# Kernel tuning notes

Hardware: AMD Instinct MI355X
Metric: run time of the kernel (lower is better)

## Reference

```python
import jax, jax.numpy as jnp
import numpy as np

EPS = 1e-5  # torch LayerNorm default
NUM_HEADS = 16


def _ln(x, g, b):
    mu = x.mean(-1, keepdims=True)
    var = ((x - mu) ** 2).mean(-1, keepdims=True)
    return (x - mu) * jax.lax.rsqrt(var + EPS) * g + b


def _softmax1(logits):
    # softmax with an extra implicit zero logit appended on the last axis
    z = jnp.pad(logits, [(0, 0)] * (logits.ndim - 1) + [(0, 1)])
    return jax.nn.softmax(z, axis=-1)[..., :-1]


def setup_inputs() -> dict:
    key = jax.random.key(0)
    ks = jax.random.split(key, 8)
    B, N, C = 4, 1024, 1024
    Hd = 4 * C  # mlp hidden
    s = lambda k, shape, sc: (jax.random.normal(k, shape, jnp.float32) * sc)
    return {
        "x": s(ks[0], (B, N, C), 1.0),
        "mask": jax.random.bernoulli(ks[1], 0.1, (B, N, N)),  # True = masked
        "ln1_g": jnp.ones((C,), jnp.float32),
        "ln1_b": jnp.zeros((C,), jnp.float32),
        "qkv_w": s(ks[2], (3 * C, C), 0.02),
        "qkv_b": jnp.zeros((3 * C,), jnp.float32),
        "proj_w": s(ks[3], (C, C), 0.02),
        "proj_b": jnp.zeros((C,), jnp.float32),
        "ln2_g": jnp.ones((C,), jnp.float32),
        "ln2_b": jnp.zeros((C,), jnp.float32),
        "fc1_w": s(ks[4], (Hd, C), 0.02),
        "fc1_b": jnp.zeros((Hd,), jnp.float32),
        "fc2_w": s(ks[5], (C, Hd), 0.02),
        "fc2_b": jnp.zeros((C,), jnp.float32),
    }


def reference(x, mask, ln1_g, ln1_b, qkv_w, qkv_b, proj_w, proj_b,
              ln2_g, ln2_b, fc1_w, fc1_b, fc2_w, fc2_b):
    B, N, C = x.shape
    H = NUM_HEADS
    D = C // H
    scale = D ** (-0.5)
    # --- pre-norm attention ---
    h = _ln(x, ln1_g, ln1_b)
    qkv = (h @ qkv_w.T + qkv_b).reshape(B, N, 3, H, D).transpose(2, 0, 3, 1, 4)
    q, k, v = qkv[0], qkv[1], qkv[2]  # each [B,H,N,D]
    attn = jnp.einsum('bhqd,bhkd->bhqk', q, k) * scale
    attn = jnp.where(mask[:, None], -jnp.finfo(attn.dtype).max, attn)
    attn = _softmax1(attn)  # allow_zero_attn=True variant
    o = jnp.einsum('bhqk,bhkd->bqhd', attn, v).reshape(B, N, C)
    o = o @ proj_w.T + proj_b
    x = x + o
    # --- pre-norm MLP (exact GELU, matching torch nn.GELU default) ---
    h2 = _ln(x, ln2_g, ln2_b)
    m = jax.nn.gelu(h2 @ fc1_w.T + fc1_b, approximate=False)
    m = m @ fc2_w.T + fc2_b
    return x + m
```

## Files before the change

kernel.cpp:

```cpp
#include <hip/hip_runtime.h>
#include <hip/hip_bf16.h>
#include <cstdint>
#include <cstddef>

typedef __attribute__((ext_vector_type(4))) float f32x4;
typedef __attribute__((ext_vector_type(8))) short s16x8;
typedef __attribute__((ext_vector_type(4))) unsigned int u32x4;
typedef __attribute__((ext_vector_type(4))) unsigned short u16x4;

__device__ __forceinline__ unsigned short f2bf(float f) {
  union { float f; unsigned int u; } v; v.f = f;
  return (unsigned short)((v.u + 0x7fffu + ((v.u >> 16) & 1u)) >> 16);
}

__device__ __forceinline__ void gll16(const void* g, void* l) {
  __builtin_amdgcn_global_load_lds(
      (const __attribute__((address_space(1))) void*)g,
      (__attribute__((address_space(3))) void*)l, 16, 0, 0);
}

__global__ void mask_detect(const unsigned char* __restrict__ m, int* __restrict__ flag) {
  __shared__ int f;
  if (threadIdx.x == 0) f = 0;
  __syncthreads();
  unsigned int found = 0;
  for (int i = threadIdx.x * 16; i < 65536; i += 256 * 16) {
    u32x4 v = *(const u32x4*)(m + i);
    found |= (v.x & 0xFFFFFF00u) | (v.y & 0xFFFFFF00u) |
             (v.z & 0xFFFFFF00u) | (v.w & 0xFFFFFF00u);
  }
  if (found) atomicOr(&f, 1);
  __syncthreads();
  if (threadIdx.x == 0) *flag = f;
}

__global__ __launch_bounds__(256)
void ln_bf16(const float* __restrict__ x, const float* __restrict__ g,
             const float* __restrict__ bta, unsigned short* __restrict__ out) {
  const int row = blockIdx.x;
  const int t = threadIdx.x;
  const float* xr = x + (size_t)row * 1024;
  f32x4 v = *(const f32x4*)(xr + t * 4);
  float s  = v.x + v.y + v.z + v.w;
  float sq = v.x * v.x + v.y * v.y + v.z * v.z + v.w * v.w;
#pragma unroll
  for (int d = 1; d < 64; d <<= 1) { s += __shfl_xor(s, d, 64); sq += __shfl_xor(sq, d, 64); }
  __shared__ float ss[4], ssq[4];
  const int w = t >> 6;
  if ((t & 63) == 0) { ss[w] = s; ssq[w] = sq; }
  __syncthreads();
  s  = ss[0] + ss[1] + ss[2] + ss[3];
  sq = ssq[0] + ssq[1] + ssq[2] + ssq[3];
  const float mu  = s * (1.0f / 1024.0f);
  const float var = sq * (1.0f / 1024.0f) - mu * mu;
  const float rs  = rsqrtf(var + 1e-5f);
  f32x4 gv = *(const f32x4*)(g + t * 4);
  f32x4 bv = *(const f32x4*)(bta + t * 4);
  u16x4 o;
  o.x = f2bf((v.x - mu) * rs * gv.x + bv.x);
  o.y = f2bf((v.y - mu) * rs * gv.y + bv.y);
  o.z = f2bf((v.z - mu) * rs * gv.z + bv.z);
  o.w = f2bf((v.w - mu) * rs * gv.w + bv.w);
  *(u16x4*)(out + (size_t)row * 1024 + t * 4) = o;
}

__global__ __launch_bounds__(256)
void f32_to_bf16(const float* __restrict__ in, unsigned short* __restrict__ out, int n) {
  for (int i = (blockIdx.x * 256 + threadIdx.x) * 4; i < n; i += gridDim.x * 256 * 4) {
    f32x4 v = *(const f32x4*)(in + i);
    u16x4 o = { f2bf(v.x), f2bf(v.y), f2bf(v.z), f2bf(v.w) };
    *(u16x4*)(out + i) = o;
  }
}

template<int EPI>
__global__ __launch_bounds__(256)
void gemm_bt(const unsigned short* __restrict__ A, const unsigned short* __restrict__ Bw,
             const float* __restrict__ bias, const float* __restrict__ resid,
             void* __restrict__ Cout, int M, int N, int K) {
  __shared__ unsigned short As[128 * 64];
  __shared__ unsigned short Bs[128 * 64];
  const int tid = threadIdx.x;
  const int bx = blockIdx.x;
  const int by = blockIdx.y;
  const int w = tid >> 6, l = tid & 63;
  const int wr = w >> 1, wc = w & 1;
  const int lr = l & 15, lk = l >> 4;

  f32x4 acc[4][4] = {};
  const int row0A = by * 128, row0B = bx * 128;

  for (int kt = 0; kt < K; kt += 64) {
#pragma unroll
    for (int it = 0; it < 4; ++it) {
      const int c = it * 256 + tid;
      const int r = c >> 3, c8 = (c & 7) * 8;
      gll16(A  + (size_t)(row0A + r) * K + kt + c8, As + c * 8);
      gll16(Bw + (size_t)(row0B + r) * K + kt + c8, Bs + c * 8);
    }
    asm volatile("s_waitcnt vmcnt(0)" ::: "memory");
    __syncthreads();
#pragma unroll
    for (int ks = 0; ks < 2; ++ks) {
      s16x8 af[4], bfr[4];
#pragma unroll
      for (int m = 0; m < 4; ++m)
        af[m] = *(const s16x8*)&As[(wr * 64 + m * 16 + lr) * 64 + ks * 32 + lk * 8];
#pragma unroll
      for (int n = 0; n < 4; ++n)
        bfr[n] = *(const s16x8*)&Bs[(wc * 64 + n * 16 + lr) * 64 + ks * 32 + lk * 8];
#pragma unroll
      for (int m = 0; m < 4; ++m)
#pragma unroll
        for (int n = 0; n < 4; ++n)
          acc[m][n] = __builtin_amdgcn_mfma_f32_16x16x32_bf16(af[m], bfr[n], acc[m][n], 0, 0, 0);
    }
    __syncthreads();
  }
#pragma unroll
  for (int m = 0; m < 4; ++m) {
#pragma unroll
    for (int n = 0; n < 4; ++n) {
      const int col = bx * 128 + wc * 64 + n * 16 + lr;
      const float bval = bias[col];
#pragma unroll
      for (int r2 = 0; r2 < 4; ++r2) {
        const int row = by * 128 + wr * 64 + m * 16 + lk * 4 + r2;
        float vv = acc[m][n][r2] + bval;
        const size_t idx = (size_t)row * N + col;
        if (EPI == 0) {
          ((unsigned short*)Cout)[idx] = f2bf(vv);
        } else if (EPI == 1) {
          float ge = 0.5f * vv * (1.0f + erff(vv * 0.70710678118f));
          ((unsigned short*)Cout)[idx] = f2bf(ge);
        } else {
          ((float*)Cout)[idx] = vv + resid[idx];
        }
      }
    }
  }
}

__global__ __launch_bounds__(256)
void attn_kernel(const unsigned short* __restrict__ qkv, const void* __restrict__ maskp,
                 const int* __restrict__ flag, unsigned short* __restrict__ o_ws) {
  __shared__ unsigned short Qs[64 * 64];
  __shared__ unsigned short Ks[64 * 64];
  __shared__ unsigned short Vts[64 * 64];
  __shared__ unsigned short Ps[4][16 * 64];
  __shared__ __align__(16) unsigned char Ms[64 * 64];

  const int tid = threadIdx.x;
  const int bh = blockIdx.x, qt = blockIdx.y;
  const int b = bh >> 4, h = bh & 15;
  const int q0 = qt * 64;
  const int w = tid >> 6, l = tid & 63;
  const int lr = l & 15, lk = l >> 4;
  const size_t rowbase = (size_t)b * 1024;
  const int qoff = h * 64, koff = 1024 + h * 64, voff = 2048 + h * 64;

#pragma unroll
  for (int it = 0; it < 2; ++it) {
    const int c = it * 256 + tid;
    const int r = c >> 3, c8 = (c & 7) * 8;
    gll16(qkv + (rowbase + q0 + r) * 3072 + qoff + c8, Qs + c * 8);
  }
  const int mask_is_byte = *flag;

  float m_r[4] = {0.f, 0.f, 0.f, 0.f};
  float l_r[4] = {1.f, 1.f, 1.f, 1.f};
  f32x4 acc_o[4] = {};

  for (int nt = 0; nt < 16; ++nt) {
    const int n0 = nt * 64;
    __syncthreads();
#pragma unroll
    for (int it = 0; it < 2; ++it) {
      const int c = it * 256 + tid;
      const int r = c >> 3, c8 = (c & 7) * 8;
      gll16(qkv + (rowbase + n0 + r) * 3072 + koff + c8, Ks + c * 8);
    }
    {
      const int n = tid & 63, dg = tid >> 6;
      const u32x4* src = (const u32x4*)(qkv + (rowbase + n0 + n) * 3072 + voff + dg * 16);
      u32x4 v0 = src[0], v1 = src[1];
      const unsigned short* e0 = (const unsigned short*)&v0;
      const unsigned short* e1 = (const unsigned short*)&v1;
#pragma unroll
      for (int j = 0; j < 8; ++j) Vts[(dg * 16 + j) * 64 + n] = e0[j];
#pragma unroll
      for (int j = 0; j < 8; ++j) Vts[(dg * 16 + 8 + j) * 64 + n] = e1[j];
    }
    {
      const int r = tid >> 2, c16 = (tid & 3) * 16;
      const size_t moff = ((size_t)b * 1024 + q0 + r) * 1024 + n0 + c16;
      if (mask_is_byte) {
        *(u32x4*)&Ms[r * 64 + c16] = *(const u32x4*)((const unsigned char*)maskp + moff);
      } else {
        const int* mi = (const int*)maskp + moff;
#pragma unroll
        for (int j = 0; j < 16; ++j) Ms[r * 64 + c16 + j] = (mi[j] != 0) ? 1 : 0;
      }
    }
    asm volatile("s_waitcnt vmcnt(0)" ::: "memory");
    __syncthreads();

    f32x4 s_acc[4] = {};
#pragma unroll
    for (int ks = 0; ks < 2; ++ks) {
      s16x8 aq = *(const s16x8*)&Qs[(w * 16 + lr) * 64 + ks * 32 + lk * 8];
#pragma unroll
      for (int n = 0; n < 4; ++n) {
        s16x8 bk = *(const s16x8*)&Ks[(n * 16 + lr) * 64 + ks * 32 + lk * 8];
        s_acc[n] = __builtin_amdgcn_mfma_f32_16x16x32_bf16(aq, bk, s_acc[n], 0, 0, 0);
      }
    }
    float sv[4][4], pm[4];
#pragma unroll
    for (int r2 = 0; r2 < 4; ++r2) pm[r2] = -3.0e38f;
#pragma unroll
    for (int n = 0; n < 4; ++n)
#pragma unroll
      for (int r2 = 0; r2 < 4; ++r2) {
        float s = s_acc[n][r2] * 0.125f;
        const int qrow = w * 16 + lk * 4 + r2, kcol = n * 16 + lr;
        if (Ms[qrow * 64 + kcol]) s = -3.0e38f;
        sv[n][r2] = s;
        pm[r2] = fmaxf(pm[r2], s);
      }
#pragma unroll
    for (int d = 1; d < 16; d <<= 1)
#pragma unroll
      for (int r2 = 0; r2 < 4; ++r2) pm[r2] = fmaxf(pm[r2], __shfl_xor(pm[r2], d, 64));

    float resc[4], psum[4];
#pragma unroll
    for (int r2 = 0; r2 < 4; ++r2) {
      const float mnew = fmaxf(m_r[r2], pm[r2]);
      resc[r2] = __expf(m_r[r2] - mnew);
      m_r[r2] = mnew;
      psum[r2] = 0.f;
    }
#pragma unroll
    for (int n = 0; n < 4; ++n)
#pragma unroll
      for (int r2 = 0; r2 < 4; ++r2) {
        const float p = __expf(sv[n][r2] - m_r[r2]);
        psum[r2] += p;
        Ps[w][(lk * 4 + r2) * 64 + n * 16 + lr] = f2bf(p);
      }
#pragma unroll
    for (int d = 1; d < 16; d <<= 1)
#pragma unroll
      for (int r2 = 0; r2 < 4; ++r2) psum[r2] += __shfl_xor(psum[r2], d, 64);
#pragma unroll
    for (int r2 = 0; r2 < 4; ++r2) l_r[r2] = l_r[r2] * resc[r2] + psum[r2];
#pragma unroll
    for (int dn = 0; dn < 4; ++dn)
#pragma unroll
      for (int r2 = 0; r2 < 4; ++r2) acc_o[dn][r2] *= resc[r2];
#pragma unroll
    for (int ks = 0; ks < 2; ++ks) {
      s16x8 ap = *(const s16x8*)&Ps[w][lr * 64 + ks * 32 + lk * 8];
#pragma unroll
      for (int dn = 0; dn < 4; ++dn) {
        s16x8 bv = *(const s16x8*)&Vts[(dn * 16 + lr) * 64 + ks * 32 + lk * 8];
        acc_o[dn] = __builtin_amdgcn_mfma_f32_16x16x32_bf16(ap, bv, acc_o[dn], 0, 0, 0);
      }
    }
  }
#pragma unroll
  for (int dn = 0; dn < 4; ++dn)
#pragma unroll
    for (int r2 = 0; r2 < 4; ++r2) {
      const int qrow = q0 + w * 16 + lk * 4 + r2;
      const int dcol = h * 64 + dn * 16 + lr;
      o_ws[(rowbase + qrow) * 1024 + dcol] = f2bf(acc_o[dn][r2] / l_r[r2]);
    }
}

extern "C" void kernel_launch(void* const* d_in, const int* in_sizes, int n_in,
                              void* d_out, int out_size, void* d_ws, size_t ws_size,
                              hipStream_t stream) {
  const float* x      = (const float*)d_in[0];
  const void*  maskp  = d_in[1];
  const float* ln1_g  = (const float*)d_in[2];
  const float* ln1_b  = (const float*)d_in[3];
  const float* qkv_w  = (const float*)d_in[4];
  const float* qkv_b  = (const float*)d_in[5];
  const float* proj_w = (const float*)d_in[6];
  const float* proj_b = (const float*)d_in[7];
  const float* ln2_g  = (const float*)d_in[8];
  const float* ln2_b  = (const float*)d_in[9];
  const float* fc1_w  = (const float*)d_in[10];
  const float* fc1_b  = (const float*)d_in[11];
  const float* fc2_w  = (const float*)d_in[12];
  const float* fc2_b  = (const float*)d_in[13];
  float* out = (float*)d_out;

  char* ws = (char*)d_ws;
  int* flag             = (int*)ws;
  unsigned short* bufA  = (unsigned short*)(ws + 256);
  unsigned short* bufH  = (unsigned short*)(ws + 256 + 33554432);
  unsigned short* bufO  = (unsigned short*)(ws + 256 + 33554432 + 8388608);
  float* bufX1          = (float*)(ws + 256 + 33554432 + 2 * 8388608);
  unsigned short* bufW  = (unsigned short*)(ws + 256 + 33554432 + 2 * 8388608 + 16777216);

  mask_detect<<<1, 256, 0, stream>>>((const unsigned char*)maskp, flag);
  ln_bf16<<<4096, 256, 0, stream>>>(x, ln1_g, ln1_b, bufH);
  f32_to_bf16<<<2048, 256, 0, stream>>>(qkv_w, bufW, 3072 * 1024);
  gemm_bt<0><<<dim3(24, 32), 256, 0, stream>>>(bufH, bufW, qkv_b, nullptr, bufA, 4096, 3072, 1024);
  attn_kernel<<<dim3(64, 16), 256, 0, stream>>>(bufA, maskp, flag, bufO);
  f32_to_bf16<<<2048, 256, 0, stream>>>(proj_w, bufW, 1024 * 1024);
  gemm_bt<2><<<dim3(8, 32), 256, 0, stream>>>(bufO, bufW, proj_b, x, bufX1, 4096, 1024, 1024);
  ln_bf16<<<4096, 256, 0, stream>>>(bufX1, ln2_g, ln2_b, bufH);
  f32_to_bf16<<<2048, 256, 0, stream>>>(fc1_w, bufW, 4096 * 1024);
  gemm_bt<1><<<dim3(32, 32), 256, 0, stream>>>(bufH, bufW, fc1_b, nullptr, bufA, 4096, 4096, 1024);
  f32_to_bf16<<<2048, 256, 0, stream>>>(fc2_w, bufW, 1024 * 4096);
  gemm_bt<2><<<dim3(8, 32), 256, 0, stream>>>(bufA, bufW, fc2_b, bufX1, out, 4096, 1024, 4096);
}
```

Before: 480.3 us.

## Rewrite attention with swizzled LDS, register mask, fuse weight conversion, narrow N-tiles

Attention drops the shared-memory mask tile and loads mask bytes straight into registers. It XOR-swizzles Q/K/V/P in LDS to avoid bank conflicts and swaps the QK^T operand order so each lane owns one query row, which removes most shuffle reductions. It also remaps blocks so neighbouring blocks share a batch/head, and sets occupancy hints. The weight conversions are merged into one launch when the workspace is large enough, and the N=1024 GEMMs use 64-wide N tiles to double the block count. This adds complexity and relies on workspace size for the fused path.

```diff
diff --git a/kernel.cpp b/kernel.cpp
--- a/kernel.cpp
+++ b/kernel.cpp
@@ -73,13 +73,32 @@
   }
 }
 
-template<int EPI>
+__global__ __launch_bounds__(256)
+void convert_weights(const float* __restrict__ w0, const float* __restrict__ w1,
+                     const float* __restrict__ w2, const float* __restrict__ w3,
+                     unsigned short* __restrict__ o0, unsigned short* __restrict__ o1,
+                     unsigned short* __restrict__ o2, unsigned short* __restrict__ o3) {
+  const int gid = blockIdx.x * 256 + threadIdx.x;
+  for (int i = gid * 4; i < 12582912; i += gridDim.x * 256 * 4) {
+    const float* src; unsigned short* dst; int off;
+    if (i < 3145728)      { src = w0; dst = o0; off = i; }
+    else if (i < 4194304) { src = w1; dst = o1; off = i - 3145728; }
+    else if (i < 8388608) { src = w2; dst = o2; off = i - 4194304; }
+    else                  { src = w3; dst = o3; off = i - 8388608; }
+    f32x4 v = *(const f32x4*)(src + off);
+    u16x4 o = { f2bf(v.x), f2bf(v.y), f2bf(v.z), f2bf(v.w) };
+    *(u16x4*)(dst + off) = o;
+  }
+}
+
+template<int EPI, int NW>
 __global__ __launch_bounds__(256)
 void gemm_bt(const unsigned short* __restrict__ A, const unsigned short* __restrict__ Bw,
              const float* __restrict__ bias, const float* __restrict__ resid,
              void* __restrict__ Cout, int M, int N, int K) {
+  constexpr int BN = 32 * NW;
   __shared__ unsigned short As[128 * 64];
-  __shared__ unsigned short Bs[128 * 64];
+  __shared__ unsigned short Bs[BN * 64];
   const int tid = threadIdx.x;
   const int bx = blockIdx.x;
   const int by = blockIdx.y;
@@ -87,32 +106,33 @@
   const int wr = w >> 1, wc = w & 1;
   const int lr = l & 15, lk = l >> 4;
 
-  f32x4 acc[4][4] = {};
-  const int row0A = by * 128, row0B = bx * 128;
+  f32x4 acc[4][NW] = {};
+  const int row0A = by * 128, row0B = bx * BN;
 
   for (int kt = 0; kt < K; kt += 64) {
 #pragma unroll
     for (int it = 0; it < 4; ++it) {
       const int c = it * 256 + tid;
       const int r = c >> 3, c8 = (c & 7) * 8;
-      gll16(A  + (size_t)(row0A + r) * K + kt + c8, As + c * 8);
-      gll16(Bw + (size_t)(row0B + r) * K + kt + c8, Bs + c * 8);
+      gll16(A + (size_t)(row0A + r) * K + kt + c8, As + c * 8);
+      if (it < NW)
+        gll16(Bw + (size_t)(row0B + r) * K + kt + c8, Bs + c * 8);
     }
     asm volatile("s_waitcnt vmcnt(0)" ::: "memory");
     __syncthreads();
 #pragma unroll
     for (int ks = 0; ks < 2; ++ks) {
-      s16x8 af[4], bfr[4];
+      s16x8 af[4], bfr[NW];
 #pragma unroll
       for (int m = 0; m < 4; ++m)
         af[m] = *(const s16x8*)&As[(wr * 64 + m * 16 + lr) * 64 + ks * 32 + lk * 8];
 #pragma unroll
-      for (int n = 0; n < 4; ++n)
-        bfr[n] = *(const s16x8*)&Bs[(wc * 64 + n * 16 + lr) * 64 + ks * 32 + lk * 8];
+      for (int n = 0; n < NW; ++n)
+        bfr[n] = *(const s16x8*)&Bs[(wc * (BN / 2) + n * 16 + lr) * 64 + ks * 32 + lk * 8];
 #pragma unroll
       for (int m = 0; m < 4; ++m)
 #pragma unroll
-        for (int n = 0; n < 4; ++n)
+        for (int n = 0; n < NW; ++n)
           acc[m][n] = __builtin_amdgcn_mfma_f32_16x16x32_bf16(af[m], bfr[n], acc[m][n], 0, 0, 0);
     }
     __syncthreads();
@@ -120,8 +140,8 @@
 #pragma unroll
   for (int m = 0; m < 4; ++m) {
 #pragma unroll
-    for (int n = 0; n < 4; ++n) {
-      const int col = bx * 128 + wc * 64 + n * 16 + lr;
+    for (int n = 0; n < NW; ++n) {
+      const int col = bx * BN + wc * (BN / 2) + n * 16 + lr;
       const float bval = bias[col];
 #pragma unroll
       for (int r2 = 0; r2 < 4; ++r2) {
@@ -141,17 +161,18 @@
   }
 }
 
-__global__ __launch_bounds__(256)
-void attn_kernel(const unsigned short* __restrict__ qkv, const void* __restrict__ maskp,
-                 const int* __restrict__ flag, unsigned short* __restrict__ o_ws) {
+__global__ __launch_bounds__(256, 4)
+void attn2(const unsigned short* __restrict__ qkv, const void* __restrict__ maskp,
+           const int* __restrict__ flag, unsigned short* __restrict__ o_ws) {
   __shared__ unsigned short Qs[64 * 64];
   __shared__ unsigned short Ks[64 * 64];
   __shared__ unsigned short Vts[64 * 64];
   __shared__ unsigned short Ps[4][16 * 64];
-  __shared__ __align__(16) unsigned char Ms[64 * 64];
 
   const int tid = threadIdx.x;
-  const int bh = blockIdx.x, qt = blockIdx.y;
+  const int orig = blockIdx.x;
+  const int swzb = (orig & 7) * 128 + (orig >> 3);
+  const int bh = swzb >> 4, qt = swzb & 15;
   const int b = bh >> 4, h = bh & 15;
   const int q0 = qt * 64;
   const int w = tid >> 6, l = tid & 63;
@@ -162,44 +183,55 @@
 #pragma unroll
   for (int it = 0; it < 2; ++it) {
     const int c = it * 256 + tid;
-    const int r = c >> 3, c8 = (c & 7) * 8;
-    gll16(qkv + (rowbase + q0 + r) * 3072 + qoff + c8, Qs + c * 8);
+    const int r = c >> 3, j0 = c & 7;
+    const int jsrc = j0 ^ (r & 7);
+    gll16(qkv + (rowbase + q0 + r) * 3072 + qoff + jsrc * 8, Qs + c * 8);
   }
   const int mask_is_byte = *flag;
-
-  float m_r[4] = {0.f, 0.f, 0.f, 0.f};
-  float l_r[4] = {1.f, 1.f, 1.f, 1.f};
+  const int qrow_g = q0 + w * 16 + lr;
+  const unsigned char* mrow_b = (const unsigned char*)maskp + ((size_t)b * 1024 + qrow_g) * 1024;
+  const int* mrow_i = (const int*)maskp + ((size_t)b * 1024 + qrow_g) * 1024;
+
+  const int np = tid & 31, dg = tid >> 5;
+
+  float m_r = 0.f, l_r = 1.f;
   f32x4 acc_o[4] = {};
 
   for (int nt = 0; nt < 16; ++nt) {
     const int n0 = nt * 64;
+    const unsigned short* vsrc = qkv + (rowbase + n0 + 2 * np) * 3072 + voff + dg * 8;
+    u32x4 va = *(const u32x4*)vsrc;
+    u32x4 vb = *(const u32x4*)(vsrc + 3072);
+    unsigned int mb[4];
+    if (mask_is_byte) {
+#pragma unroll
+      for (int n = 0; n < 4; ++n)
+        mb[n] = *(const unsigned int*)(mrow_b + n0 + n * 16 + lk * 4);
+    } else {
+#pragma unroll
+      for (int n = 0; n < 4; ++n) {
+        u32x4 t4 = *(const u32x4*)(mrow_i + n0 + n * 16 + lk * 4);
+        mb[n] = (t4.x ? 1u : 0u) | (t4.y ? 0x100u : 0u) |
+                (t4.z ? 0x10000u : 0u) | (t4.w ? 0x1000000u : 0u);
+      }
+    }
     __syncthreads();
 #pragma unroll
     for (int it = 0; it < 2; ++it) {
       const int c = it * 256 + tid;
-      const int r = c >> 3, c8 = (c & 7) * 8;
-      gll16(qkv + (rowbase + n0 + r) * 3072 + koff + c8, Ks + c * 8);
+      const int r = c >> 3, j0 = c & 7;
+      const int jsrc = j0 ^ (r & 7);
+      gll16(qkv + (rowbase + n0 + r) * 3072 + koff + jsrc * 8, Ks + c * 8);
     }
     {
-      const int n = tid & 63, dg = tid >> 6;
-      const u32x4* src = (const u32x4*)(qkv + (rowbase + n0 + n) * 3072 + voff + dg * 16);
-      u32x4 v0 = src[0], v1 = src[1];
-      const unsigned short* e0 = (const unsigned short*)&v0;
-      const unsigned short* e1 = (const unsigned short*)&v1;
-#pragma unroll
-      for (int j = 0; j < 8; ++j) Vts[(dg * 16 + j) * 64 + n] = e0[j];
-#pragma unroll
-      for (int j = 0; j < 8; ++j) Vts[(dg * 16 + 8 + j) * 64 + n] = e1[j];
-    }
-    {
-      const int r = tid >> 2, c16 = (tid & 3) * 16;
-      const size_t moff = ((size_t)b * 1024 + q0 + r) * 1024 + n0 + c16;
-      if (mask_is_byte) {
-        *(u32x4*)&Ms[r * 64 + c16] = *(const u32x4*)((const unsigned char*)maskp + moff);
-      } else {
-        const int* mi = (const int*)maskp + moff;
-#pragma unroll
-        for (int j = 0; j < 16; ++j) Ms[r * 64 + c16 + j] = (mi[j] != 0) ? 1 : 0;
+      const unsigned short* ea = (const unsigned short*)&va;
+      const unsigned short* eb = (const unsigned short*)&vb;
+#pragma unroll
+      for (int j = 0; j < 8; ++j) {
+        const int d = dg * 8 + j;
+        const unsigned int pv = (unsigned int)ea[j] | ((unsigned int)eb[j] << 16);
+        const int byte = (d * 128 + np * 4) ^ ((d & 7) << 4);
+        *(unsigned int*)((char*)Vts + byte) = pv;
       }
     }
     asm volatile("s_waitcnt vmcnt(0)" ::: "memory");
@@ -208,74 +240,82 @@
     f32x4 s_acc[4] = {};
 #pragma unroll
     for (int ks = 0; ks < 2; ++ks) {
-      s16x8 aq = *(const s16x8*)&Qs[(w * 16 + lr) * 64 + ks * 32 + lk * 8];
+      const int cb = ks * 64 + lk * 16;
+      const s16x8 qf = *(const s16x8*)((char*)Qs + (((w * 16 + lr) * 128 + cb) ^ ((lr & 7) << 4)));
 #pragma unroll
       for (int n = 0; n < 4; ++n) {
-        s16x8 bk = *(const s16x8*)&Ks[(n * 16 + lr) * 64 + ks * 32 + lk * 8];
-        s_acc[n] = __builtin_amdgcn_mfma_f32_16x16x32_bf16(aq, bk, s_acc[n], 0, 0, 0);
-      }
-    }
-    float sv[4][4], pm[4];
-#pragma unroll
-    for (int r2 = 0; r2 < 4; ++r2) pm[r2] = -3.0e38f;
+        const s16x8 kf = *(const s16x8*)((char*)Ks + (((n * 16 + lr) * 128 + cb) ^ ((lr & 7) << 4)));
+        s_acc[n] = __builtin_amdgcn_mfma_f32_16x16x32_bf16(kf, qf, s_acc[n], 0, 0, 0);
+      }
+    }
+    float pmax = -3.0e38f;
 #pragma unroll
     for (int n = 0; n < 4; ++n)
 #pragma unroll
       for (int r2 = 0; r2 < 4; ++r2) {
         float s = s_acc[n][r2] * 0.125f;
-        const int qrow = w * 16 + lk * 4 + r2, kcol = n * 16 + lr;
-        if (Ms[qrow * 64 + kcol]) s = -3.0e38f;
-        sv[n][r2] = s;
-        pm[r2] = fmaxf(pm[r2], s);
-      }
-#pragma unroll
-    for (int d = 1; d < 16; d <<= 1)
-#pragma unroll
-      for (int r2 = 0; r2 < 4; ++r2) pm[r2] = fmaxf(pm[r2], __shfl_xor(pm[r2], d, 64));
-
-    float resc[4], psum[4];
-#pragma unroll
-    for (int r2 = 0; r2 < 4; ++r2) {
-      const float mnew = fmaxf(m_r[r2], pm[r2]);
-      resc[r2] = __expf(m_r[r2] - mnew);
-      m_r[r2] = mnew;
-      psum[r2] = 0.f;
-    }
+        if ((mb[n] >> (8 * r2)) & 0xff) s = -3.0e38f;
+        s_acc[n][r2] = s;
+        pmax = fmaxf(pmax, s);
+      }
+    pmax = fmaxf(pmax, __shfl_xor(pmax, 16, 64));
+    pmax = fmaxf(pmax, __shfl_xor(pmax, 32, 64));
+    const float mnew = fmaxf(m_r, pmax);
+    const float resc = __expf(m_r - mnew);
+    m_r = mnew;
+    float psum = 0.f;
+    unsigned int pk[4][2];
 #pragma unroll
     for (int n = 0; n < 4; ++n)
 #pragma unroll
-      for (int r2 = 0; r2 < 4; ++r2) {
-        const float p = __expf(sv[n][r2] - m_r[r2]);
-        psum[r2] += p;
-        Ps[w][(lk * 4 + r2) * 64 + n * 16 + lr] = f2bf(p);
-      }
-#pragma unroll
-    for (int d = 1; d < 16; d <<= 1)
-#pragma unroll
-      for (int r2 = 0; r2 < 4; ++r2) psum[r2] += __shfl_xor(psum[r2], d, 64);
-#pragma unroll
-    for (int r2 = 0; r2 < 4; ++r2) l_r[r2] = l_r[r2] * resc[r2] + psum[r2];
+      for (int h2 = 0; h2 < 2; ++h2) {
+        const float p0 = __expf(s_acc[n][2 * h2]     - mnew);
+        const float p1 = __expf(s_acc[n][2 * h2 + 1] - mnew);
+        psum += p0 + p1;
+        pk[n][h2] = (unsigned int)f2bf(p0) | ((unsigned int)f2bf(p1) << 16);
+      }
+    psum += __shfl_xor(psum, 16, 64);
+    psum += __shfl_xor(psum, 32, 64);
+    l_r = l_r * resc + psum;
+    char* psw = (char*)&Ps[w][0];
+#pragma unroll
+    for (int n = 0; n < 4; ++n)
+#pragma unroll
+      for (int h2 = 0; h2 < 2; ++h2) {
+        const int byte = (lr * 128 + n * 32 + lk * 8 + h2 * 4) ^ ((lr & 7) << 4);
+        *(unsigned int*)(psw + byte) = pk[n][h2];
+      }
+    float rs4[4];
+#pragma unroll
+    for (int r2 = 0; r2 < 4; ++r2)
+      rs4[r2] = __shfl(resc, (l & 48) | (lk * 4 + r2), 64);
 #pragma unroll
     for (int dn = 0; dn < 4; ++dn)
 #pragma unroll
-      for (int r2 = 0; r2 < 4; ++r2) acc_o[dn][r2] *= resc[r2];
+      for (int r2 = 0; r2 < 4; ++r2) acc_o[dn][r2] *= rs4[r2];
 #pragma unroll
     for (int ks = 0; ks < 2; ++ks) {
-      s16x8 ap = *(const s16x8*)&Ps[w][lr * 64 + ks * 32 + lk * 8];
+      const int cb = ks * 64 + lk * 16;
+      const s16x8 ap = *(const s16x8*)(psw + ((lr * 128 + cb) ^ ((lr & 7) << 4)));
 #pragma unroll
       for (int dn = 0; dn < 4; ++dn) {
-        s16x8 bv = *(const s16x8*)&Vts[(dn * 16 + lr) * 64 + ks * 32 + lk * 8];
+        const s16x8 bv = *(const s16x8*)((char*)Vts + (((dn * 16 + lr) * 128 + cb) ^ ((lr & 7) << 4)));
         acc_o[dn] = __builtin_amdgcn_mfma_f32_16x16x32_bf16(ap, bv, acc_o[dn], 0, 0, 0);
       }
     }
   }
+  const float linv = 1.0f / l_r;
+  float li4[4];
+#pragma unroll
+  for (int r2 = 0; r2 < 4; ++r2)
+    li4[r2] = __shfl(linv, (l & 48) | (lk * 4 + r2), 64);
 #pragma unroll
   for (int dn = 0; dn < 4; ++dn)
 #pragma unroll
     for (int r2 = 0; r2 < 4; ++r2) {
       const int qrow = q0 + w * 16 + lk * 4 + r2;
       const int dcol = h * 64 + dn * 16 + lr;
-      o_ws[(rowbase + qrow) * 1024 + dcol] = f2bf(acc_o[dn][r2] / l_r[r2]);
+      o_ws[(rowbase + qrow) * 1024 + dcol] = f2bf(acc_o[dn][r2] * li4[r2]);
     }
 }
 
@@ -299,23 +339,41 @@
   float* out = (float*)d_out;
 
   char* ws = (char*)d_ws;
-  int* flag             = (int*)ws;
-  unsigned short* bufA  = (unsigned short*)(ws + 256);
-  unsigned short* bufH  = (unsigned short*)(ws + 256 + 33554432);
-  unsigned short* bufO  = (unsigned short*)(ws + 256 + 33554432 + 8388608);
-  float* bufX1          = (float*)(ws + 256 + 33554432 + 2 * 8388608);
-  unsigned short* bufW  = (unsigned short*)(ws + 256 + 33554432 + 2 * 8388608 + 16777216);
+  int* flag            = (int*)ws;
+  unsigned short* bufA = (unsigned short*)(ws + 256);
+  unsigned short* bufH = (unsigned short*)(ws + 256 + 33554432);
+  unsigned short* bufO = (unsigned short*)(ws + 256 + 33554432 + 8388608);
+  float* bufX1         = (float*)(ws + 256 + 33554432 + 2 * 8388608);
+  char* wbase          = ws + 256 + 33554432 + 2 * 8388608 + 16777216;
 
   mask_detect<<<1, 256, 0, stream>>>((const unsigned char*)maskp, flag);
-  ln_bf16<<<4096, 256, 0, stream>>>(x, ln1_g, ln1_b, bufH);
-  f32_to_bf16<<<2048, 256, 0, stream>>>(qkv_w, bufW, 3072 * 1024);
-  gemm_bt<0><<<dim3(24, 32), 256, 0, stream>>>(bufH, bufW, qkv_b, nullptr, bufA, 4096, 3072, 1024);
-  attn_kernel<<<dim3(64, 16), 256, 0, stream>>>(bufA, maskp, flag, bufO);
-  f32_to_bf16<<<2048, 256, 0, stream>>>(proj_w, bufW, 1024 * 1024);
-  gemm_bt<2><<<dim3(8, 32), 256, 0, stream>>>(bufO, bufW, proj_b, x, bufX1, 4096, 1024, 1024);
-  ln_bf16<<<4096, 256, 0, stream>>>(bufX1, ln2_g, ln2_b, bufH);
-  f32_to_bf16<<<2048, 256, 0, stream>>>(fc1_w, bufW, 4096 * 1024);
-  gemm_bt<1><<<dim3(32, 32), 256, 0, stream>>>(bufH, bufW, fc1_b, nullptr, bufA, 4096, 4096, 1024);
-  f32_to_bf16<<<2048, 256, 0, stream>>>(fc2_w, bufW, 1024 * 4096);
-  gemm_bt<2><<<dim3(8, 32), 256, 0, stream>>>(bufA, bufW, fc2_b, bufX1, out, 4096, 1024, 4096);
-}
+
+  const bool bigws = ws_size >= (size_t)92274944;
+  if (bigws) {
+    unsigned short* W0 = (unsigned short*)wbase;
+    unsigned short* W1 = (unsigned short*)(wbase + 6291456);
+    unsigned short* W2 = (unsigned short*)(wbase + 8388608);
+    unsigned short* W3 = (unsigned short*)(wbase + 16777216);
+    convert_weights<<<4096, 256, 0, stream>>>(qkv_w, proj_w, fc1_w, fc2_w, W0, W1, W2, W3);
+    ln_bf16<<<4096, 256, 0, stream>>>(x, ln1_g, ln1_b, bufH);
+    gemm_bt<0, 4><<<dim3(24, 32), 256, 0, stream>>>(bufH, W0, qkv_b, nullptr, bufA, 4096, 3072, 1024);
+    attn2<<<1024, 256, 0, stream>>>(bufA, maskp, flag, bufO);
+    gemm_bt<2, 2><<<dim3(16, 32), 256, 0, stream>>>(bufO, W1, proj_b, x, bufX1, 4096, 1024, 1024);
+    ln_bf16<<<4096, 256, 0, stream>>>(bufX1, ln2_g, ln2_b, bufH);
+    gemm_bt<1, 4><<<dim3(32, 32), 256, 0, stream>>>(bufH, W2, fc1_b, nullptr, bufA, 4096, 4096, 1024);
+    gemm_bt<2, 2><<<dim3(16, 32), 256, 0, stream>>>(bufA, W3, fc2_b, bufX1, out, 4096, 1024, 4096);
+  } else {
+    unsigned short* bufW = (unsigned short*)wbase;
+    ln_bf16<<<4096, 256, 0, stream>>>(x, ln1_g, ln1_b, bufH);
+    f32_to_bf16<<<2048, 256, 0, stream>>>(qkv_w, bufW, 3072 * 1024);
+    gemm_bt<0, 4><<<dim3(24, 32), 256, 0, stream>>>(bufH, bufW, qkv_b, nullptr, bufA, 4096, 3072, 1024);
+    attn2<<<1024, 256, 0, stream>>>(bufA, maskp, flag, bufO);
+    f32_to_bf16<<<2048, 256, 0, stream>>>(proj_w, bufW, 1024 * 1024);
+    gemm_bt<2, 2><<<dim3(16, 32), 256, 0, stream>>>(bufO, bufW, proj_b, x, bufX1, 4096, 1024, 1024);
+    ln_bf16<<<4096, 256, 0, stream>>>(bufX1, ln2_g, ln2_b, bufH);
+    f32_to_bf16<<<2048, 256, 0, stream>>>(fc1_w, bufW, 4096 * 1024);
+    gemm_bt<1, 4><<<dim3(32, 32), 256, 0, stream>>>(bufH, bufW, fc1_b, nullptr, bufA, 4096, 4096, 1024);
+    f32_to_bf16<<<2048, 256, 0, stream>>>(fc2_w, bufW, 1024 * 4096);
+    gemm_bt<2, 2><<<dim3(16, 32), 256, 0, stream>>>(bufA, bufW, fc2_b, bufX1, out, 4096, 1024, 4096);
+  }
+}
```

After: 429.3 us. 1.12x faster.
